# Kernel optimization log

Measured on AMD Instinct MI355X. Metric: run time of the kernel, lower is better.

The kernel has to match this reference:

```python
import jax, jax.numpy as jnp
import numpy as np

H, W = 480, 640
NUM_CLASSES = 3
SKIP = 5            # skip_pixels: stride between voting pixels
GRID = 8            # stride of Hough accumulator bins
LABEL_THRESHOLD = 5
INLIER_THRESHOLD = 0.5
VOTING_THRESHOLD = 0.3


def setup_inputs():
    key = jax.random.key(0)
    k1, k2, k3, k4 = jax.random.split(key, 4)
    bottom_label = jax.random.randint(k1, (1, H, W), 0, NUM_CLASSES).astype(jnp.int32)
    bottom_vertex = jax.random.normal(k2, (1, NUM_CLASSES * 3, H, W), jnp.float32)
    bottom_meta_data = jax.random.normal(k3, (1, 10), jnp.float32)
    extents = jax.random.normal(k4, (NUM_CLASSES, 3), jnp.float32)
    return {"bottom_label": bottom_label, "bottom_vertex": bottom_vertex,
            "bottom_meta_data": bottom_meta_data, "extents": extents}


def _hough_voting(bottom_label, bottom_vertex, bottom_meta_data, extents):
    label = bottom_label[0]                                   # [H,W] int
    vert = bottom_vertex[0].reshape(NUM_CLASSES, 3, H, W)     # per-class (ux,uy,dist)

    # voter pixels on a SKIP-strided grid
    vy, vx = jnp.meshgrid(jnp.arange(0, H, SKIP), jnp.arange(0, W, SKIP), indexing="ij")
    vy = vy.reshape(-1)
    vx = vx.reshape(-1)                                       # [V]
    vl = label[vy, vx]                                        # voter class labels [V]
    d = vert[vl, :, vy, vx]                                   # [V,3] gather own-class prediction
    ux, uy, dist = d[:, 0], d[:, 1], d[:, 2]

    # Hough bin centers on a GRID-strided grid
    by, bx = jnp.meshgrid(jnp.arange(GRID // 2, H, GRID), jnp.arange(GRID // 2, W, GRID), indexing="ij")
    by = by.reshape(-1).astype(jnp.float32)
    bx = bx.reshape(-1).astype(jnp.float32)                   # [B]

    # per (voter, bin) agreement between predicted direction and vector to bin
    ddx = bx[None, :] - vx[:, None].astype(jnp.float32)       # [V,B]
    ddy = by[None, :] - vy[:, None].astype(jnp.float32)
    inv_n = jax.lax.rsqrt(ddx * ddx + ddy * ddy + 1e-6)
    cos = (ddx * ux[:, None] + ddy * uy[:, None]) * inv_n     # [V,B]
    w = jnp.where((cos > INLIER_THRESHOLD) & (vl[:, None] > 0), 1.0, 0.0)

    # scatter votes into per-class Hough space (class 0 = background, masked above)
    hough = jax.ops.segment_sum(w, vl, num_segments=NUM_CLASSES)                 # [C,B]
    dsum = jax.ops.segment_sum(w * dist[:, None], vl, num_segments=NUM_CLASSES)  # [C,B]
    counts = jax.ops.segment_sum(jnp.ones_like(vl, jnp.float32), vl, num_segments=NUM_CLASSES)

    # peak detection per class
    peak = jnp.argmax(hough, axis=1)                          # [C]
    votes = jnp.take_along_axis(hough, peak[:, None], axis=1)[:, 0]
    depth = jnp.take_along_axis(dsum, peak[:, None], axis=1)[:, 0] / jnp.maximum(votes, 1.0)
    cx = bx[peak]
    cy = by[peak]
    score = votes / jnp.maximum(counts, 1.0)
    valid = (counts > LABEL_THRESHOLD) & (score > VOTING_THRESHOLD)

    # project object extents through camera intrinsics at estimated depth -> box size
    fx = bottom_meta_data[0, 0]
    fy = bottom_meta_data[0, 4]
    diag = jnp.sqrt(jnp.sum(extents * extents, axis=1))       # [C]
    safe_z = jnp.maximum(jnp.abs(depth), 1e-3)
    bw = jnp.abs(diag * fx) / safe_z
    bh = jnp.abs(diag * fy) / safe_z

    cls = jnp.arange(NUM_CLASSES, dtype=jnp.float32)
    rois = jnp.stack([cls, cx - bw / 2, cy - bh / 2, cx + bw / 2, cy + bh / 2,
                      score * valid.astype(jnp.float32)], axis=1)  # [C,6]
    return rois, hough


def reference(bottom_label, bottom_vertex, bottom_meta_data, extents):
    return _hough_voting(bottom_label, bottom_vertex, bottom_meta_data, extents)
```

## Files before the change

### kernel.cpp

```cpp
#include <hip/hip_runtime.h>

#define HH 480
#define WW 640
#define HW (HH * WW)
#define NC 3
#define NVX 128
#define NVY 96
#define NV (NVX * NVY)
#define NBX 80
#define NBY 60
#define NB (NBX * NBY)
#define NSL 48
#define BINBLOCKS ((NB + 255) / 256)

__global__ void vote_fused(const int* __restrict__ label,
                           const float* __restrict__ vert,
                           float4* __restrict__ partial,
                           int2* __restrict__ sliceCounts) {
    __shared__ float4 shA[256];
    __shared__ float  shD[256];
    __shared__ int sw1[4], sw2[4];

    const int tid = threadIdx.x;
    const int slice = blockIdx.y;
    const int i = slice * 256 + tid;
    const int iy = i >> 7;
    const int ix = i & (NVX - 1);
    const int pix = (5 * iy) * WW + 5 * ix;
    const int vl = label[pix];
    const float* base = vert + (size_t)(vl * 3) * HW + pix;
    const float ux = base[0];
    const float uy = base[HW];
    const float dist = base[(size_t)2 * HW];

    const int lane = tid & 63, w = tid >> 6;
    const unsigned long long lt = (1ull << lane) - 1ull;
    const unsigned long long m1 = __ballot(vl == 1);
    const unsigned long long m2 = __ballot(vl == 2);
    if (lane == 0) { sw1[w] = __popcll(m1); sw2[w] = __popcll(m2); }
    __syncthreads();
    const int n1 = sw1[0] + sw1[1] + sw1[2] + sw1[3];
    const int n2 = sw2[0] + sw2[1] + sw2[2] + sw2[3];
    int o1 = 0, o2 = 0;
    for (int k = 0; k < w; ++k) { o1 += sw1[k]; o2 += sw2[k]; }
    if (vl == 1) {
        int p = o1 + __popcll(m1 & lt);
        shA[p] = make_float4((float)(5 * ix), (float)(5 * iy), 2.0f * ux, 2.0f * uy);
        shD[p] = dist;
    } else if (vl == 2) {
        int p = n1 + o2 + __popcll(m2 & lt);
        shA[p] = make_float4((float)(5 * ix), (float)(5 * iy), 2.0f * ux, 2.0f * uy);
        shD[p] = dist;
    }
    if (blockIdx.x == 0 && tid == 0) sliceCounts[slice] = make_int2(n1, n2);
    __syncthreads();

    const int b = blockIdx.x * 256 + tid;
    const float bxf = (float)(4 + 8 * (b % NBX));
    const float byf = (float)(4 + 8 * (b / NBX));
    float h1 = 0.f, d1 = 0.f, h2 = 0.f, d2 = 0.f;

    const int e1 = __builtin_amdgcn_readfirstlane(n1);
    const int e2 = __builtin_amdgcn_readfirstlane(n1 + n2);

#define PAIR_BODY(HACC, DACC)                                                        \
    {                                                                                \
        float4 a = shA[j];                                                           \
        float ddx = bxf - a.x;                                                       \
        float ddy = byf - a.y;                                                       \
        float nx  = __builtin_fmaf(ddx, ddx, __builtin_fmaf(ddy, ddy, 1e-6f));       \
        float dot = __builtin_fmaf(ddx, a.z, ddy * a.w);                             \
        float s   = __builtin_fmaf(dot, dot, -nx);                                   \
        bool v = (dot > 0.0f) & (s > 0.0f);                                          \
        if (__builtin_expect((dot > 0.0f) && (fabsf(s) < nx * 8e-5f), 0)) {          \
            float nxe  = __fadd_rn(__fadd_rn(__fmul_rn(ddx, ddx),                    \
                                             __fmul_rn(ddy, ddy)), 1e-6f);           \
            float inve = __fdiv_rn(1.0f, __fsqrt_rn(nxe));                           \
            float dote = __fadd_rn(__fmul_rn(ddx, 0.5f * a.z),                       \
                                   __fmul_rn(ddy, 0.5f * a.w));                      \
            v = __fmul_rn(dote, inve) > 0.5f;                                        \
        }                                                                            \
        float m = v ? 1.0f : 0.0f;                                                   \
        HACC += m;                                                                   \
        DACC = __builtin_fmaf(m, shD[j], DACC);                                      \
    }

#pragma unroll 4
    for (int j = 0; j < e1; ++j) PAIR_BODY(h1, d1)
#pragma unroll 4
    for (int j = e1; j < e2; ++j) PAIR_BODY(h2, d2)
#undef PAIR_BODY

    if (b < NB) partial[slice * NB + b] = make_float4(h1, d1, h2, d2);
}

__global__ void reduce_vote(const float4* __restrict__ partial,
                            float* __restrict__ hough,
                            float* __restrict__ dsum,
                            unsigned long long* __restrict__ cand) {
    __shared__ unsigned long long sk1[256], sk2[256];
    const int tid = threadIdx.x;
    const int b = blockIdx.x * 256 + tid;
    unsigned long long k1 = 0ull, k2 = 0ull;
    if (b < NB) {
        float h1 = 0.f, d1 = 0.f, h2 = 0.f, d2 = 0.f;
#pragma unroll 8
        for (int s = 0; s < NSL; ++s) {
            float4 p = partial[s * NB + b];
            h1 += p.x; d1 += p.y; h2 += p.z; d2 += p.w;
        }
        hough[b] = 0.0f;
        hough[NB + b] = h1;
        hough[2 * NB + b] = h2;
        dsum[b] = d1;
        dsum[NB + b] = d2;
        const unsigned long long idx = (unsigned long long)(unsigned)(NB - 1 - b);
        k1 = ((unsigned long long)__float_as_uint(h1) << 32) | idx;
        k2 = ((unsigned long long)__float_as_uint(h2) << 32) | idx;
    }
    sk1[tid] = k1; sk2[tid] = k2;
    __syncthreads();
    for (int s = 128; s > 0; s >>= 1) {
        if (tid < s) {
            if (sk1[tid + s] > sk1[tid]) sk1[tid] = sk1[tid + s];
            if (sk2[tid + s] > sk2[tid]) sk2[tid] = sk2[tid + s];
        }
        __syncthreads();
    }
    if (tid == 0) {
        cand[blockIdx.x * 2]     = sk1[0];
        cand[blockIdx.x * 2 + 1] = sk2[0];
    }
}

__global__ void finalize(const unsigned long long* __restrict__ cand,
                         const int2* __restrict__ sliceCounts,
                         const float* __restrict__ dsum,
                         const float* __restrict__ meta,
                         const float* __restrict__ extents,
                         float* __restrict__ rois) {
    const int tid = threadIdx.x;
    unsigned long long k1 = (tid < BINBLOCKS) ? cand[tid * 2]     : 0ull;
    unsigned long long k2 = (tid < BINBLOCKS) ? cand[tid * 2 + 1] : 0ull;
    int cn1 = 0, cn2 = 0;
    if (tid < NSL) { int2 c = sliceCounts[tid]; cn1 = c.x; cn2 = c.y; }
    for (int off = 32; off > 0; off >>= 1) {
        unsigned long long o1 = __shfl_xor(k1, off);
        unsigned long long o2 = __shfl_xor(k2, off);
        if (o1 > k1) k1 = o1;
        if (o2 > k2) k2 = o2;
        cn1 += __shfl_xor(cn1, off);
        cn2 += __shfl_xor(cn2, off);
    }
    if (tid < NC) {
        const int c = tid;
        float votes; int peak;
        if (c == 0) { votes = 0.0f; peak = 0; }
        else {
            unsigned long long k = (c == 1) ? k1 : k2;
            votes = __uint_as_float((unsigned)(k >> 32));
            peak = NB - 1 - (int)(k & 0xffffffffull);
        }
        const float cntf = (c == 0) ? (float)(NV - cn1 - cn2)
                                    : ((c == 1) ? (float)cn1 : (float)cn2);
        const float ds = (c == 0) ? 0.0f : dsum[(c - 1) * NB + peak];
        const float depth = __fdiv_rn(ds, fmaxf(votes, 1.0f));
        const float cx = (float)(4 + 8 * (peak % NBX));
        const float cy = (float)(4 + 8 * (peak / NBX));
        const float score = __fdiv_rn(votes, fmaxf(cntf, 1.0f));
        const int valid = (cntf > 5.0f) && (score > 0.3f);
        const float fx = meta[0], fy = meta[4];
        const float e0 = extents[c * 3 + 0];
        const float e1 = extents[c * 3 + 1];
        const float e2 = extents[c * 3 + 2];
        const float diag = __fsqrt_rn(__fadd_rn(
            __fadd_rn(__fmul_rn(e0, e0), __fmul_rn(e1, e1)), __fmul_rn(e2, e2)));
        const float sz = fmaxf(fabsf(depth), 0.001f);
        const float bw = __fdiv_rn(fabsf(__fmul_rn(diag, fx)), sz);
        const float bh = __fdiv_rn(fabsf(__fmul_rn(diag, fy)), sz);
        rois[c * 6 + 0] = (float)c;
        rois[c * 6 + 1] = cx - bw * 0.5f;
        rois[c * 6 + 2] = cy - bh * 0.5f;
        rois[c * 6 + 3] = cx + bw * 0.5f;
        rois[c * 6 + 4] = cy + bh * 0.5f;
        rois[c * 6 + 5] = valid ? score : 0.0f;
    }
}

extern "C" void kernel_launch(void* const* d_in, const int* in_sizes, int n_in,
                              void* d_out, int out_size, void* d_ws, size_t ws_size,
                              hipStream_t stream) {
    const int* label = (const int*)d_in[0];
    const float* vert = (const float*)d_in[1];
    const float* meta = (const float*)d_in[2];
    const float* extents = (const float*)d_in[3];
    float* out = (float*)d_out;

    char* ws = (char*)d_ws;
    float4* partial = (float4*)ws;
    float* dsum = (float*)(ws + (size_t)NSL * NB * 16);
    unsigned long long* cand =
        (unsigned long long*)(ws + (size_t)NSL * NB * 16 + 2 * NB * 4);
    int2* sliceCounts =
        (int2*)(ws + (size_t)NSL * NB * 16 + 2 * NB * 4 + 2 * BINBLOCKS * 8);

    float* hough = out + NC * 6;

    vote_fused<<<dim3(BINBLOCKS, NSL), 256, 0, stream>>>(label, vert, partial, sliceCounts);
    reduce_vote<<<BINBLOCKS, 256, 0, stream>>>(partial, hough, dsum, cand);
    finalize<<<1, 64, 0, stream>>>(cand, sliceCounts, dsum, meta, extents, out);
}
```

Measured before the change: 97.96 us.

## Process two voter slices per block and fuse finalize into reduce via ticket

Each vote block now loads and compacts two 256-voter slices, so there are 24 voter groups instead of 48. This halves the partial-sum buffer written and then re-read by the reduction. The separate single-block finalize launch is folded into the reduce kernel with a last-block-done atomic ticket, saving one kernel launch. In exchange, each vote block does twice the pair work and uses more shared memory, and the grid has half as many blocks to spread across the CUs.

```diff
diff --git a/kernel.cpp b/kernel.cpp
--- a/kernel.cpp
+++ b/kernel.cpp
@@ -10,49 +10,67 @@
 #define NBX 80
 #define NBY 60
 #define NB (NBX * NBY)
-#define NSL 48
+#define NGRP 24
 #define BINBLOCKS ((NB + 255) / 256)
 
 __global__ void vote_fused(const int* __restrict__ label,
                            const float* __restrict__ vert,
                            float4* __restrict__ partial,
-                           int2* __restrict__ sliceCounts) {
-    __shared__ float4 shA[256];
-    __shared__ float  shD[256];
-    __shared__ int sw1[4], sw2[4];
+                           int2* __restrict__ groupCounts,
+                           unsigned int* __restrict__ ticket) {
+    __shared__ float4 shA[512];
+    __shared__ float  shD[512];
+    __shared__ int sw1[2][4], sw2[2][4];
 
     const int tid = threadIdx.x;
-    const int slice = blockIdx.y;
-    const int i = slice * 256 + tid;
-    const int iy = i >> 7;
-    const int ix = i & (NVX - 1);
-    const int pix = (5 * iy) * WW + 5 * ix;
-    const int vl = label[pix];
-    const float* base = vert + (size_t)(vl * 3) * HW + pix;
-    const float ux = base[0];
-    const float uy = base[HW];
-    const float dist = base[(size_t)2 * HW];
-
     const int lane = tid & 63, w = tid >> 6;
     const unsigned long long lt = (1ull << lane) - 1ull;
-    const unsigned long long m1 = __ballot(vl == 1);
-    const unsigned long long m2 = __ballot(vl == 2);
-    if (lane == 0) { sw1[w] = __popcll(m1); sw2[w] = __popcll(m2); }
-    __syncthreads();
-    const int n1 = sw1[0] + sw1[1] + sw1[2] + sw1[3];
-    const int n2 = sw2[0] + sw2[1] + sw2[2] + sw2[3];
-    int o1 = 0, o2 = 0;
-    for (int k = 0; k < w; ++k) { o1 += sw1[k]; o2 += sw2[k]; }
-    if (vl == 1) {
-        int p = o1 + __popcll(m1 & lt);
-        shA[p] = make_float4((float)(5 * ix), (float)(5 * iy), 2.0f * ux, 2.0f * uy);
-        shD[p] = dist;
-    } else if (vl == 2) {
-        int p = n1 + o2 + __popcll(m2 & lt);
-        shA[p] = make_float4((float)(5 * ix), (float)(5 * iy), 2.0f * ux, 2.0f * uy);
-        shD[p] = dist;
-    }
-    if (blockIdx.x == 0 && tid == 0) sliceCounts[slice] = make_int2(n1, n2);
+    const int grp = blockIdx.y;
+
+    int vls[2]; float uxs[2], uys[2], dss[2], pxs[2], pys[2]; int r1[2], r2[2];
+#pragma unroll
+    for (int ss = 0; ss < 2; ++ss) {
+        const int i = (grp * 2 + ss) * 256 + tid;
+        const int iy = i >> 7;
+        const int ix = i & (NVX - 1);
+        const int pix = (5 * iy) * WW + 5 * ix;
+        const int vl = label[pix];
+        const float* base = vert + (size_t)(vl * 3) * HW + pix;
+        vls[ss] = vl;
+        uxs[ss] = base[0];
+        uys[ss] = base[HW];
+        dss[ss] = base[(size_t)2 * HW];
+        pxs[ss] = (float)(5 * ix);
+        pys[ss] = (float)(5 * iy);
+        const unsigned long long m1 = __ballot(vl == 1);
+        const unsigned long long m2 = __ballot(vl == 2);
+        if (lane == 0) { sw1[ss][w] = __popcll(m1); sw2[ss][w] = __popcll(m2); }
+        r1[ss] = __popcll(m1 & lt);
+        r2[ss] = __popcll(m2 & lt);
+    }
+    __syncthreads();
+    int n1t[2], n2t[2];
+#pragma unroll
+    for (int ss = 0; ss < 2; ++ss) {
+        n1t[ss] = sw1[ss][0] + sw1[ss][1] + sw1[ss][2] + sw1[ss][3];
+        n2t[ss] = sw2[ss][0] + sw2[ss][1] + sw2[ss][2] + sw2[ss][3];
+        int o1 = 0, o2 = 0;
+        for (int k = 0; k < w; ++k) { o1 += sw1[ss][k]; o2 += sw2[ss][k]; }
+        const int basep = ss * 256;
+        if (vls[ss] == 1) {
+            const int p = basep + o1 + r1[ss];
+            shA[p] = make_float4(pxs[ss], pys[ss], 2.0f * uxs[ss], 2.0f * uys[ss]);
+            shD[p] = dss[ss];
+        } else if (vls[ss] == 2) {
+            const int p = basep + n1t[ss] + o2 + r2[ss];
+            shA[p] = make_float4(pxs[ss], pys[ss], 2.0f * uxs[ss], 2.0f * uys[ss]);
+            shD[p] = dss[ss];
+        }
+    }
+    if (blockIdx.x == 0 && tid == 0) {
+        groupCounts[grp] = make_int2(n1t[0] + n1t[1], n2t[0] + n2t[1]);
+        if (grp == 0) *ticket = 0u;
+    }
     __syncthreads();
 
     const int b = blockIdx.x * 256 + tid;
@@ -60,8 +78,10 @@
     const float byf = (float)(4 + 8 * (b / NBX));
     float h1 = 0.f, d1 = 0.f, h2 = 0.f, d2 = 0.f;
 
-    const int e1 = __builtin_amdgcn_readfirstlane(n1);
-    const int e2 = __builtin_amdgcn_readfirstlane(n1 + n2);
+    const int a1e = __builtin_amdgcn_readfirstlane(n1t[0]);
+    const int a2e = __builtin_amdgcn_readfirstlane(n1t[0] + n2t[0]);
+    const int b1e = __builtin_amdgcn_readfirstlane(256 + n1t[1]);
+    const int b2e = __builtin_amdgcn_readfirstlane(256 + n1t[1] + n2t[1]);
 
 #define PAIR_BODY(HACC, DACC)                                                        \
     {                                                                                \
@@ -86,26 +106,36 @@
     }
 
 #pragma unroll 4
-    for (int j = 0; j < e1; ++j) PAIR_BODY(h1, d1)
-#pragma unroll 4
-    for (int j = e1; j < e2; ++j) PAIR_BODY(h2, d2)
+    for (int j = 0; j < a1e; ++j) PAIR_BODY(h1, d1)
+#pragma unroll 4
+    for (int j = 256; j < b1e; ++j) PAIR_BODY(h1, d1)
+#pragma unroll 4
+    for (int j = a1e; j < a2e; ++j) PAIR_BODY(h2, d2)
+#pragma unroll 4
+    for (int j = b1e; j < b2e; ++j) PAIR_BODY(h2, d2)
 #undef PAIR_BODY
 
-    if (b < NB) partial[slice * NB + b] = make_float4(h1, d1, h2, d2);
+    if (b < NB) partial[grp * NB + b] = make_float4(h1, d1, h2, d2);
 }
 
-__global__ void reduce_vote(const float4* __restrict__ partial,
-                            float* __restrict__ hough,
-                            float* __restrict__ dsum,
-                            unsigned long long* __restrict__ cand) {
+__global__ void reduce_finalize(const float4* __restrict__ partial,
+                                const int2* __restrict__ groupCounts,
+                                float* __restrict__ hough,
+                                float* __restrict__ dsum,
+                                unsigned long long* __restrict__ cand,
+                                unsigned int* __restrict__ ticket,
+                                const float* __restrict__ meta,
+                                const float* __restrict__ extents,
+                                float* __restrict__ rois) {
     __shared__ unsigned long long sk1[256], sk2[256];
+    __shared__ int sdone;
     const int tid = threadIdx.x;
     const int b = blockIdx.x * 256 + tid;
     unsigned long long k1 = 0ull, k2 = 0ull;
     if (b < NB) {
         float h1 = 0.f, d1 = 0.f, h2 = 0.f, d2 = 0.f;
-#pragma unroll 8
-        for (int s = 0; s < NSL; ++s) {
+#pragma unroll 6
+        for (int s = 0; s < NGRP; ++s) {
             float4 p = partial[s * NB + b];
             h1 += p.x; d1 += p.y; h2 += p.z; d2 += p.w;
         }
@@ -130,25 +160,23 @@
     if (tid == 0) {
         cand[blockIdx.x * 2]     = sk1[0];
         cand[blockIdx.x * 2 + 1] = sk2[0];
-    }
-}
-
-__global__ void finalize(const unsigned long long* __restrict__ cand,
-                         const int2* __restrict__ sliceCounts,
-                         const float* __restrict__ dsum,
-                         const float* __restrict__ meta,
-                         const float* __restrict__ extents,
-                         float* __restrict__ rois) {
-    const int tid = threadIdx.x;
-    unsigned long long k1 = (tid < BINBLOCKS) ? cand[tid * 2]     : 0ull;
-    unsigned long long k2 = (tid < BINBLOCKS) ? cand[tid * 2 + 1] : 0ull;
+        __threadfence();
+        unsigned prev = atomicAdd(ticket, 1u);
+        sdone = (prev == (unsigned)(BINBLOCKS - 1)) ? 1 : 0;
+    }
+    __syncthreads();
+    if (sdone == 0 || tid >= 64) return;
+
+    __threadfence();
+    unsigned long long f1 = (tid < BINBLOCKS) ? cand[tid * 2]     : 0ull;
+    unsigned long long f2 = (tid < BINBLOCKS) ? cand[tid * 2 + 1] : 0ull;
     int cn1 = 0, cn2 = 0;
-    if (tid < NSL) { int2 c = sliceCounts[tid]; cn1 = c.x; cn2 = c.y; }
+    if (tid < NGRP) { int2 c = groupCounts[tid]; cn1 = c.x; cn2 = c.y; }
     for (int off = 32; off > 0; off >>= 1) {
-        unsigned long long o1 = __shfl_xor(k1, off);
-        unsigned long long o2 = __shfl_xor(k2, off);
-        if (o1 > k1) k1 = o1;
-        if (o2 > k2) k2 = o2;
+        unsigned long long o1 = __shfl_xor(f1, off);
+        unsigned long long o2 = __shfl_xor(f2, off);
+        if (o1 > f1) f1 = o1;
+        if (o2 > f2) f2 = o2;
         cn1 += __shfl_xor(cn1, off);
         cn2 += __shfl_xor(cn2, off);
     }
@@ -157,7 +185,7 @@
         float votes; int peak;
         if (c == 0) { votes = 0.0f; peak = 0; }
         else {
-            unsigned long long k = (c == 1) ? k1 : k2;
+            unsigned long long k = (c == 1) ? f1 : f2;
             votes = __uint_as_float((unsigned)(k >> 32));
             peak = NB - 1 - (int)(k & 0xffffffffull);
         }
@@ -198,15 +226,19 @@
 
     char* ws = (char*)d_ws;
     float4* partial = (float4*)ws;
-    float* dsum = (float*)(ws + (size_t)NSL * NB * 16);
-    unsigned long long* cand =
-        (unsigned long long*)(ws + (size_t)NSL * NB * 16 + 2 * NB * 4);
-    int2* sliceCounts =
-        (int2*)(ws + (size_t)NSL * NB * 16 + 2 * NB * 4 + 2 * BINBLOCKS * 8);
+    size_t off = (size_t)NGRP * NB * 16;
+    float* dsum = (float*)(ws + off);
+    off += (size_t)2 * NB * 4;
+    unsigned long long* cand = (unsigned long long*)(ws + off);
+    off += (size_t)2 * BINBLOCKS * 8;
+    int2* groupCounts = (int2*)(ws + off);
+    off += (size_t)NGRP * 8;
+    unsigned int* ticket = (unsigned int*)(ws + off);
 
     float* hough = out + NC * 6;
 
-    vote_fused<<<dim3(BINBLOCKS, NSL), 256, 0, stream>>>(label, vert, partial, sliceCounts);
-    reduce_vote<<<BINBLOCKS, 256, 0, stream>>>(partial, hough, dsum, cand);
-    finalize<<<1, 64, 0, stream>>>(cand, sliceCounts, dsum, meta, extents, out);
+    vote_fused<<<dim3(BINBLOCKS, NGRP), 256, 0, stream>>>(label, vert, partial,
+                                                          groupCounts, ticket);
+    reduce_finalize<<<BINBLOCKS, 256, 0, stream>>>(partial, groupCounts, hough, dsum,
+                                                   cand, ticket, meta, extents, out);
 }
```

Measured after the change: 109.7 us. 12.0% more time.

## Split voter loop across thread pairs and fuse finalize into reduce via ticket

Applied to the files above, without the earlier changes.

Each bin is now handled by two threads that stride over the compacted voter list, and their partial sums are combined with a lane shuffle. This doubles the grid of vote blocks (38 instead of 19 along x) so the GPU has more parallelism. The separate finalize launch is folded into the reduce kernel: the last block to finish, detected with an atomic ticket reset by the vote kernel, does the peak and ROI computation. This saves one launch but adds atomic and fence overhead, and the extra shuffles add work per bin.

```diff
diff --git a/kernel.cpp b/kernel.cpp
--- a/kernel.cpp
+++ b/kernel.cpp
@@ -10,19 +10,24 @@
 #define NBX 80
 #define NBY 60
 #define NB (NBX * NBY)
-#define NSL 48
+#define NSLICE 48
+#define NBB 38
 #define BINBLOCKS ((NB + 255) / 256)
 
 __global__ void vote_fused(const int* __restrict__ label,
                            const float* __restrict__ vert,
-                           float4* __restrict__ partial,
-                           int2* __restrict__ sliceCounts) {
+                           float2* __restrict__ partial2,
+                           int2* __restrict__ sliceCounts,
+                           unsigned int* __restrict__ ticket) {
     __shared__ float4 shA[256];
     __shared__ float  shD[256];
     __shared__ int sw1[4], sw2[4];
 
     const int tid = threadIdx.x;
+    const int lane = tid & 63, w = tid >> 6;
+    const unsigned long long lt = (1ull << lane) - 1ull;
     const int slice = blockIdx.y;
+
     const int i = slice * 256 + tid;
     const int iy = i >> 7;
     const int ix = i & (NVX - 1);
@@ -33,8 +38,6 @@
     const float uy = base[HW];
     const float dist = base[(size_t)2 * HW];
 
-    const int lane = tid & 63, w = tid >> 6;
-    const unsigned long long lt = (1ull << lane) - 1ull;
     const unsigned long long m1 = __ballot(vl == 1);
     const unsigned long long m2 = __ballot(vl == 2);
     if (lane == 0) { sw1[w] = __popcll(m1); sw2[w] = __popcll(m2); }
@@ -44,20 +47,24 @@
     int o1 = 0, o2 = 0;
     for (int k = 0; k < w; ++k) { o1 += sw1[k]; o2 += sw2[k]; }
     if (vl == 1) {
-        int p = o1 + __popcll(m1 & lt);
+        const int p = o1 + __popcll(m1 & lt);
         shA[p] = make_float4((float)(5 * ix), (float)(5 * iy), 2.0f * ux, 2.0f * uy);
         shD[p] = dist;
     } else if (vl == 2) {
-        int p = n1 + o2 + __popcll(m2 & lt);
+        const int p = n1 + o2 + __popcll(m2 & lt);
         shA[p] = make_float4((float)(5 * ix), (float)(5 * iy), 2.0f * ux, 2.0f * uy);
         shD[p] = dist;
     }
-    if (blockIdx.x == 0 && tid == 0) sliceCounts[slice] = make_int2(n1, n2);
-    __syncthreads();
-
-    const int b = blockIdx.x * 256 + tid;
-    const float bxf = (float)(4 + 8 * (b % NBX));
-    const float byf = (float)(4 + 8 * (b / NBX));
+    if (blockIdx.x == 0 && tid == 0) {
+        sliceCounts[slice] = make_int2(n1, n2);
+        if (slice == 0) *ticket = 0u;
+    }
+    __syncthreads();
+
+    const int bin = blockIdx.x * 128 + (tid >> 1);
+    const int half = tid & 1;
+    const float bxf = (float)(4 + 8 * (bin % NBX));
+    const float byf = (float)(4 + 8 * (bin / NBX));
     float h1 = 0.f, d1 = 0.f, h2 = 0.f, d2 = 0.f;
 
     const int e1 = __builtin_amdgcn_readfirstlane(n1);
@@ -86,26 +93,39 @@
     }
 
 #pragma unroll 4
-    for (int j = 0; j < e1; ++j) PAIR_BODY(h1, d1)
+    for (int j = half; j < e1; j += 2) PAIR_BODY(h1, d1)
 #pragma unroll 4
-    for (int j = e1; j < e2; ++j) PAIR_BODY(h2, d2)
+    for (int j = e1 + half; j < e2; j += 2) PAIR_BODY(h2, d2)
 #undef PAIR_BODY
 
-    if (b < NB) partial[slice * NB + b] = make_float4(h1, d1, h2, d2);
+    h1 += __shfl_xor(h1, 1);
+    d1 += __shfl_xor(d1, 1);
+    h2 += __shfl_xor(h2, 1);
+    d2 += __shfl_xor(d2, 1);
+    if (bin < NB) {
+        const float2 val = half ? make_float2(h2, d2) : make_float2(h1, d1);
+        partial2[(size_t)(slice * NB + bin) * 2 + half] = val;
+    }
 }
 
-__global__ void reduce_vote(const float4* __restrict__ partial,
-                            float* __restrict__ hough,
-                            float* __restrict__ dsum,
-                            unsigned long long* __restrict__ cand) {
+__global__ void reduce_finalize(const float4* __restrict__ partial,
+                                const int2* __restrict__ sliceCounts,
+                                float* __restrict__ hough,
+                                float* __restrict__ dsum,
+                                unsigned long long* __restrict__ cand,
+                                unsigned int* __restrict__ ticket,
+                                const float* __restrict__ meta,
+                                const float* __restrict__ extents,
+                                float* __restrict__ rois) {
     __shared__ unsigned long long sk1[256], sk2[256];
+    __shared__ int sdone;
     const int tid = threadIdx.x;
     const int b = blockIdx.x * 256 + tid;
     unsigned long long k1 = 0ull, k2 = 0ull;
     if (b < NB) {
         float h1 = 0.f, d1 = 0.f, h2 = 0.f, d2 = 0.f;
 #pragma unroll 8
-        for (int s = 0; s < NSL; ++s) {
+        for (int s = 0; s < NSLICE; ++s) {
             float4 p = partial[s * NB + b];
             h1 += p.x; d1 += p.y; h2 += p.z; d2 += p.w;
         }
@@ -130,25 +150,23 @@
     if (tid == 0) {
         cand[blockIdx.x * 2]     = sk1[0];
         cand[blockIdx.x * 2 + 1] = sk2[0];
-    }
-}
-
-__global__ void finalize(const unsigned long long* __restrict__ cand,
-                         const int2* __restrict__ sliceCounts,
-                         const float* __restrict__ dsum,
-                         const float* __restrict__ meta,
-                         const float* __restrict__ extents,
-                         float* __restrict__ rois) {
-    const int tid = threadIdx.x;
-    unsigned long long k1 = (tid < BINBLOCKS) ? cand[tid * 2]     : 0ull;
-    unsigned long long k2 = (tid < BINBLOCKS) ? cand[tid * 2 + 1] : 0ull;
+        __threadfence();
+        unsigned prev = atomicAdd(ticket, 1u);
+        sdone = (prev == (unsigned)(BINBLOCKS - 1)) ? 1 : 0;
+    }
+    __syncthreads();
+    if (sdone == 0 || tid >= 64) return;
+
+    __threadfence();
+    unsigned long long f1 = (tid < BINBLOCKS) ? cand[tid * 2]     : 0ull;
+    unsigned long long f2 = (tid < BINBLOCKS) ? cand[tid * 2 + 1] : 0ull;
     int cn1 = 0, cn2 = 0;
-    if (tid < NSL) { int2 c = sliceCounts[tid]; cn1 = c.x; cn2 = c.y; }
+    if (tid < NSLICE) { int2 c = sliceCounts[tid]; cn1 = c.x; cn2 = c.y; }
     for (int off = 32; off > 0; off >>= 1) {
-        unsigned long long o1 = __shfl_xor(k1, off);
-        unsigned long long o2 = __shfl_xor(k2, off);
-        if (o1 > k1) k1 = o1;
-        if (o2 > k2) k2 = o2;
+        unsigned long long o1 = __shfl_xor(f1, off);
+        unsigned long long o2 = __shfl_xor(f2, off);
+        if (o1 > f1) f1 = o1;
+        if (o2 > f2) f2 = o2;
         cn1 += __shfl_xor(cn1, off);
         cn2 += __shfl_xor(cn2, off);
     }
@@ -157,7 +175,7 @@
         float votes; int peak;
         if (c == 0) { votes = 0.0f; peak = 0; }
         else {
-            unsigned long long k = (c == 1) ? k1 : k2;
+            unsigned long long k = (c == 1) ? f1 : f2;
             votes = __uint_as_float((unsigned)(k >> 32));
             peak = NB - 1 - (int)(k & 0xffffffffull);
         }
@@ -197,16 +215,21 @@
     float* out = (float*)d_out;
 
     char* ws = (char*)d_ws;
-    float4* partial = (float4*)ws;
-    float* dsum = (float*)(ws + (size_t)NSL * NB * 16);
-    unsigned long long* cand =
-        (unsigned long long*)(ws + (size_t)NSL * NB * 16 + 2 * NB * 4);
-    int2* sliceCounts =
-        (int2*)(ws + (size_t)NSL * NB * 16 + 2 * NB * 4 + 2 * BINBLOCKS * 8);
+    float2* partial2 = (float2*)ws;
+    size_t off = (size_t)NSLICE * NB * 16;
+    float* dsum = (float*)(ws + off);
+    off += (size_t)2 * NB * 4;
+    unsigned long long* cand = (unsigned long long*)(ws + off);
+    off += (size_t)2 * BINBLOCKS * 8;
+    int2* sliceCounts = (int2*)(ws + off);
+    off += (size_t)NSLICE * 8;
+    unsigned int* ticket = (unsigned int*)(ws + off);
 
     float* hough = out + NC * 6;
 
-    vote_fused<<<dim3(BINBLOCKS, NSL), 256, 0, stream>>>(label, vert, partial, sliceCounts);
-    reduce_vote<<<BINBLOCKS, 256, 0, stream>>>(partial, hough, dsum, cand);
-    finalize<<<1, 64, 0, stream>>>(cand, sliceCounts, dsum, meta, extents, out);
+    vote_fused<<<dim3(NBB, NSLICE), 256, 0, stream>>>(label, vert, partial2,
+                                                      sliceCounts, ticket);
+    reduce_finalize<<<BINBLOCKS, 256, 0, stream>>>((const float4*)partial2, sliceCounts,
+                                                   hough, dsum, cand, ticket,
+                                                   meta, extents, out);
 }
```

After: 93.30 us. 4.8% less time.
